# Optimization experiments

Measured on AMD Instinct MI355X. Metric: run time of the kernel, lower is better.

The kernel has to match this reference:

```python
import jax, jax.numpy as jnp
import numpy as np

B, S, D = 2, 2048, 2048
H = 16
HD = D // H
FF = 8192
EPS = 1e-5


def _layer_norm(x, g, b):
    mu = jnp.mean(x, axis=-1, keepdims=True)
    var = jnp.mean(jnp.square(x - mu), axis=-1, keepdims=True)
    return (x - mu) * jax.lax.rsqrt(var + EPS) * g + b


def setup_inputs() -> dict:
    key = jax.random.key(0)
    ks = jax.random.split(key, 8)
    s = 0.02
    return {
        "x": jax.random.normal(ks[0], (B, S, D), dtype=jnp.float32),
        "ln1_g": jnp.ones((D,), jnp.float32),
        "ln1_b": jnp.zeros((D,), jnp.float32),
        "qkv_w": jax.random.normal(ks[1], (D, 3 * D), dtype=jnp.float32) * s,
        "qkv_b": jnp.zeros((3 * D,), jnp.float32),
        "out_w": jax.random.normal(ks[2], (D, D), dtype=jnp.float32) * s,
        "out_b": jnp.zeros((D,), jnp.float32),
        "ln2_g": jnp.ones((D,), jnp.float32),
        "ln2_b": jnp.zeros((D,), jnp.float32),
        "w1": jax.random.normal(ks[3], (D, FF), dtype=jnp.float32) * s,
        "b1": jnp.zeros((FF,), jnp.float32),
        "w2": jax.random.normal(ks[4], (FF, D), dtype=jnp.float32) * s,
        "b2": jnp.zeros((D,), jnp.float32),
    }


def reference(x, ln1_g, ln1_b, qkv_w, qkv_b, out_w, out_b, ln2_g, ln2_b, w1, b1, w2, b2):
    # --- attention sub-block (pre-norm) ---
    residual = x
    h = _layer_norm(x, ln1_g, ln1_b)
    qkv = h @ qkv_w + qkv_b                      # [B,S,3D]
    q, k, v = jnp.split(qkv, 3, axis=-1)
    # [B,S,D] -> [B,H,S,HD]
    q = q.reshape(B, S, H, HD).transpose(0, 2, 1, 3)
    k = k.reshape(B, S, H, HD).transpose(0, 2, 1, 3)
    v = v.reshape(B, S, H, HD).transpose(0, 2, 1, 3)
    scores = jnp.einsum("bhqd,bhkd->bhqk", q, k)  # [B,H,S,S]
    causal = jnp.triu(jnp.ones((S, S), dtype=bool), k=1)
    scores = jnp.where(causal[None, None], -jnp.inf, scores)
    attn = jax.nn.softmax(scores / np.sqrt(HD).astype(np.float32), axis=-1)
    av = jnp.einsum("bhqk,bhkd->bhqd", attn, v)   # [B,H,S,HD]
    av = av.transpose(0, 2, 1, 3).reshape(B, S, D)
    x = residual + (av @ out_w + out_b)
    # --- FFN sub-block (pre-norm) ---
    residual = x
    h = _layer_norm(x, ln2_g, ln2_b)
    h = jax.nn.gelu(h @ w1 + b1, approximate=False)
    x = residual + (h @ w2 + b2)
    return x
```

## Files before the change

kernel.cpp:

```cpp
#include <hip/hip_runtime.h>
#include <hip/hip_bf16.h>

#define B_  2
#define S_  2048
#define D_  2048
#define H_  16
#define HD_ 128
#define FF_ 8192

typedef __bf16 bf16x8 __attribute__((ext_vector_type(8)));
typedef float  f32x4  __attribute__((ext_vector_type(4)));
typedef unsigned short u16;
typedef u16 u16x8 __attribute__((ext_vector_type(8)));
typedef unsigned uv4 __attribute__((ext_vector_type(4)));

__device__ __forceinline__ u16 f2bf(float f) {
    union { float f; unsigned u; } c; c.f = f;
    unsigned u = c.u;
    u += 0x7fffu + ((u >> 16) & 1u);
    return (u16)(u >> 16);
}

__device__ __forceinline__ void gld16(void* lds, const void* g) {
    __builtin_amdgcn_global_load_lds(
        (const __attribute__((address_space(1))) unsigned int*)g,
        (__attribute__((address_space(3))) unsigned int*)lds,
        16, 0, 0);
}

__device__ __forceinline__ bf16x8 dsr16(const u16* p) {
    unsigned a = (unsigned)(unsigned long long)
                 (const __attribute__((address_space(3))) u16*)p;
    uv4 r;
    asm volatile("ds_read_b128 %0, %1" : "=v"(r) : "v"(a));
    union { uv4 u; bf16x8 b; } c; c.u = r;
    return c.b;
}

__global__ __launch_bounds__(256)
void ln_kernel(const float* __restrict__ x, const float* __restrict__ g,
               const float* __restrict__ bb, u16* __restrict__ out)
{
    int row = blockIdx.x, tid = threadIdx.x;
    const float4* xr = (const float4*)(x + (size_t)row * D_);
    float4 a = xr[tid], c = xr[tid + 256];
    float s  = a.x + a.y + a.z + a.w + c.x + c.y + c.z + c.w;
    float s2 = a.x*a.x + a.y*a.y + a.z*a.z + a.w*a.w
             + c.x*c.x + c.y*c.y + c.z*c.z + c.w*c.w;
    #pragma unroll
    for (int off = 32; off > 0; off >>= 1) {
        s  += __shfl_down(s,  off, 64);
        s2 += __shfl_down(s2, off, 64);
    }
    __shared__ float red[16];
    __shared__ float mr[2];
    int wid = tid >> 6, lane = tid & 63;
    if (lane == 0) { red[wid] = s; red[8 + wid] = s2; }
    __syncthreads();
    if (tid == 0) {
        float ts = red[0] + red[1] + red[2] + red[3];
        float t2 = red[8] + red[9] + red[10] + red[11];
        float mu = ts * (1.0f / D_);
        float var = t2 * (1.0f / D_) - mu * mu;
        mr[0] = mu; mr[1] = rsqrtf(var + 1e-5f);
    }
    __syncthreads();
    float mu = mr[0], rstd = mr[1];
    const float4* gg = (const float4*)g;
    const float4* bv = (const float4*)bb;
    float4 g0 = gg[tid], g1 = gg[tid + 256];
    float4 b0 = bv[tid], b1 = bv[tid + 256];
    u16* orow = out + (size_t)row * D_;
    ushort4 o0, o1;
    o0.x = f2bf((a.x - mu) * rstd * g0.x + b0.x);
    o0.y = f2bf((a.y - mu) * rstd * g0.y + b0.y);
    o0.z = f2bf((a.z - mu) * rstd * g0.z + b0.z);
    o0.w = f2bf((a.w - mu) * rstd * g0.w + b0.w);
    o1.x = f2bf((c.x - mu) * rstd * g1.x + b1.x);
    o1.y = f2bf((c.y - mu) * rstd * g1.y + b1.y);
    o1.z = f2bf((c.z - mu) * rstd * g1.z + b1.z);
    o1.w = f2bf((c.w - mu) * rstd * g1.w + b1.w);
    *(ushort4*)&orow[tid * 4]         = o0;
    *(ushort4*)&orow[(tid + 256) * 4] = o1;
}

__global__ __launch_bounds__(256)
void tcvt_kernel(const float* __restrict__ W, u16* __restrict__ WT, int K, int N)
{
    __shared__ float t[32][33];
    int n0 = blockIdx.x << 5, k0 = blockIdx.y << 5;
    int tx = threadIdx.x & 31, ty = threadIdx.x >> 5;
    #pragma unroll
    for (int i = 0; i < 32; i += 8)
        t[ty + i][tx] = W[(size_t)(k0 + ty + i) * N + n0 + tx];
    __syncthreads();
    #pragma unroll
    for (int i = 0; i < 32; i += 8)
        WT[(size_t)(n0 + ty + i) * K + k0 + tx] = f2bf(t[tx][ty + i]);
}

template<int EPI>
__global__ __launch_bounds__(512, 2)
void gemm_kernel(const u16* __restrict__ A, const u16* __restrict__ BT,
                 const float* __restrict__ bias, const float* __restrict__ res,
                 void* __restrict__ outv, int M, int N, int K)
{
    __shared__ u16 ldsA[3 * 8192];
    __shared__ u16 ldsB[3 * 16384];
    (void)M;

    int tid = threadIdx.x;
    int wid = tid >> 6, lane = tid & 63;
    int wm = wid >> 2, wn = wid & 3;
    int quad = lane >> 4, l16 = lane & 15;

    int nwg = (int)gridDim.x;
    int swz = ((int)blockIdx.x & 7) * (nwg >> 3) + ((int)blockIdx.x >> 3);
    int mt = swz & 31;
    int nt = swz >> 5;
    int m0 = mt << 7, n0 = nt << 8;

    int lo3 = (tid & 7) ^ ((tid >> 3) & 7);
    int rS  = ((tid >> 3) << 1) | (lo3 >> 2);
    int cS  = (lo3 & 3) << 3;
    const u16* gA  = A  + (size_t)(m0 + rS) * K + cS;
    const u16* gB0 = BT + (size_t)(n0 + rS) * K + cS;
    const u16* gB1 = gB0 + (size_t)128 * K;

    int slot   = (((l16 & 1) << 2) | quad) ^ (l16 >> 1);
    int laneRd = (l16 >> 1) * 64 + slot * 8;
    int aRd = wm * 2048 + laneRd;
    int bRd = wn * 2048 + laneRd;

    f32x4 acc[4][4] = {};

    auto stA = [&](int b, int ks, int kofs) {
        gld16(ldsA + b * 8192 + ks * 4096 + wid * 512, gA + kofs);
    };
    auto stB = [&](int b, int ks, int kofs) {
        gld16(ldsB + b * 16384 + ks * 8192 + wid * 512, gB0 + kofs);
        gld16(ldsB + b * 16384 + ks * 8192 + 4096 + wid * 512, gB1 + kofs);
    };
    auto phase = [&](int bt, int ks, int stg, int kofs, bool vm) {
        stA(stg, ks, kofs);
        stB(stg, ks, kofs);
        const u16* ap = ldsA + bt * 8192 + ks * 4096 + aRd;
        const u16* bp = ldsB + bt * 16384 + ks * 8192 + bRd;
        bf16x8 af0 = dsr16(ap);
        bf16x8 af1 = dsr16(ap + 512);
        bf16x8 af2 = dsr16(ap + 1024);
        bf16x8 af3 = dsr16(ap + 1536);
        bf16x8 bf0 = dsr16(bp);
        bf16x8 bf1 = dsr16(bp + 512);
        bf16x8 bf2 = dsr16(bp + 1024);
        bf16x8 bf3 = dsr16(bp + 1536);
        __builtin_amdgcn_s_barrier();
        asm volatile("s_waitcnt lgkmcnt(0)" ::: "memory");
        __builtin_amdgcn_sched_barrier(0);
        __builtin_amdgcn_s_setprio(1);
        acc[0][0] = __builtin_amdgcn_mfma_f32_16x16x32_bf16(af0, bf0, acc[0][0], 0, 0, 0);
        acc[0][1] = __builtin_amdgcn_mfma_f32_16x16x32_bf16(af0, bf1, acc[0][1], 0, 0, 0);
        acc[0][2] = __builtin_amdgcn_mfma_f32_16x16x32_bf16(af0, bf2, acc[0][2], 0, 0, 0);
        acc[0][3] = __builtin_amdgcn_mfma_f32_16x16x32_bf16(af0, bf3, acc[0][3], 0, 0, 0);
        acc[1][0] = __builtin_amdgcn_mfma_f32_16x16x32_bf16(af1, bf0, acc[1][0], 0, 0, 0);
        acc[1][1] = __builtin_amdgcn_mfma_f32_16x16x32_bf16(af1, bf1, acc[1][1], 0, 0, 0);
        acc[1][2] = __builtin_amdgcn_mfma_f32_16x16x32_bf16(af1, bf2, acc[1][2], 0, 0, 0);
        acc[1][3] = __builtin_amdgcn_mfma_f32_16x16x32_bf16(af1, bf3, acc[1][3], 0, 0, 0);
        acc[2][0] = __builtin_amdgcn_mfma_f32_16x16x32_bf16(af2, bf0, acc[2][0], 0, 0, 0);
        acc[2][1] = __builtin_amdgcn_mfma_f32_16x16x32_bf16(af2, bf1, acc[2][1], 0, 0, 0);
        acc[2][2] = __builtin_amdgcn_mfma_f32_16x16x32_bf16(af2, bf2, acc[2][2], 0, 0, 0);
        acc[2][3] = __builtin_amdgcn_mfma_f32_16x16x32_bf16(af2, bf3, acc[2][3], 0, 0, 0);
        acc[3][0] = __builtin_amdgcn_mfma_f32_16x16x32_bf16(af3, bf0, acc[3][0], 0, 0, 0);
        acc[3][1] = __builtin_amdgcn_mfma_f32_16x16x32_bf16(af3, bf1, acc[3][1], 0, 0, 0);
        acc[3][2] = __builtin_amdgcn_mfma_f32_16x16x32_bf16(af3, bf2, acc[3][2], 0, 0, 0);
        acc[3][3] = __builtin_amdgcn_mfma_f32_16x16x32_bf16(af3, bf3, acc[3][3], 0, 0, 0);
        __builtin_amdgcn_sched_barrier(0);
        __builtin_amdgcn_s_setprio(0);
        if (vm) asm volatile("s_waitcnt vmcnt(6)" ::: "memory");
        __builtin_amdgcn_s_barrier();
    };

    int nkt = K >> 6;
    stA(0, 0, 0);  stB(0, 0, 0);
    stA(0, 1, 32); stB(0, 1, 32);
    stA(1, 0, 64); stB(1, 0, 64);
    stA(1, 1, 96); stB(1, 1, 96);
    asm volatile("s_waitcnt vmcnt(6)" ::: "memory");
    __builtin_amdgcn_s_barrier();

    int cur = 0;
    for (int t = 0; t < nkt; ++t) {
        int stg = cur - 1; if (stg < 0) stg = 2;
        int tp = t + 2; if (tp > nkt - 1) tp = nkt - 1;
        int kofs = tp << 6;
        phase(cur, 0, stg, kofs,      false);
        phase(cur, 1, stg, kofs + 32, true);
        cur = cur + 1; if (cur > 2) cur = 0;
    }
    asm volatile("s_waitcnt vmcnt(0)" ::: "memory");

    u16*   outb = (u16*)outv;
    float* outf = (float*)outv;
    int colb = n0 + wn * 64, rowb = m0 + wm * 64;
    #pragma unroll
    for (int j = 0; j < 4; j++) {
        int col = colb + j * 16 + l16;
        float bv = bias[col];
        #pragma unroll
        for (int i = 0; i < 4; i++) {
            int row0 = rowb + i * 16 + (quad << 2);
            #pragma unroll
            for (int r = 0; r < 4; r++) {
                float v = acc[i][j][r] + bv;
                size_t idx = (size_t)(row0 + r) * N + col;
                if (EPI == 2) {
                    outf[idx] = v + res[idx];
                } else {
                    if (EPI == 1) v = 0.5f * v * (1.0f + erff(v * 0.70710678118654752f));
                    outb[idx] = f2bf(v);
                }
            }
        }
    }
}

__global__ __launch_bounds__(256, 2)
void attn_kernel(const u16* __restrict__ qkv, u16* __restrict__ av)
{
    __shared__ u16 ldsK[4][64][32];
    __shared__ unsigned ldsVT[128][36];
    __shared__ u16 ldsP[4][32][72];
    int tid = threadIdx.x, wid = tid >> 6, lane = tid & 63;
    int quad = lane >> 4, l16 = lane & 15;
    int bh = blockIdx.y, b = bh >> 4, h = bh & 15;
    int qx = gridDim.x - 1 - blockIdx.x;
    int q0 = qx << 7;
    const u16* base = qkv + (size_t)b * S_ * (3 * D_);

    bf16x8 aq[2][4];
    #pragma unroll
    for (int set = 0; set < 2; set++) {
        int qrow = q0 + set * 64 + wid * 16 + l16;
        const u16* qp = base + (size_t)qrow * (3 * D_) + h * HD_;
        #pragma unroll
        for (int kk = 0; kk < 4; kk++)
            aq[set][kk] = *(const bf16x8*)(qp + kk * 32 + quad * 8);
    }

    float m_i[2][4], l_i[2][4];
    f32x4 oacc[2][8] = {};
    #pragma unroll
    for (int s = 0; s < 2; s++)
        #pragma unroll
        for (int r = 0; r < 4; r++) { m_i[s][r] = -1e30f; l_i[s][r] = 0.f; }

    const float scale = 0.088388347648318447f;
    int ntile = 2 * qx + 2;
    for (int jt = 0; jt < ntile; jt++) {
        int j0 = jt << 6;
        #pragma unroll
        for (int j = 0; j < 4; j++) {
            int c = wid * 4 + j;
            int kk = c >> 2, kb = c & 3;
            int key = (kb << 4) + (lane >> 2);
            const u16* g = base + (size_t)(j0 + key) * (3 * D_) + D_ + h * HD_
                         + kk * 32 + ((lane & 3) << 3);
            gld16((u16*)ldsK + c * 512, g);
        }
        {
            int kp = lane & 31, dhalf = lane >> 5;
            #pragma unroll
            for (int p = 0; p < 2; p++) {
                int doff = wid * 32 + p * 16 + dhalf * 8;
                const u16* g0 = base + (size_t)(j0 + 2 * kp) * (3 * D_)
                              + 2 * D_ + h * HD_ + doff;
                u16x8 v0 = *(const u16x8*)g0;
                u16x8 v1 = *(const u16x8*)(g0 + 3 * D_);
                #pragma unroll
                for (int k = 0; k < 8; k++)
                    ldsVT[doff + k][kp] = (unsigned)v0[k] | ((unsigned)v1[k] << 16);
            }
        }
        __syncthreads();
        f32x4 sacc[2][4] = {};
        #pragma unroll
        for (int kk = 0; kk < 4; kk++)
            #pragma unroll
            for (int n = 0; n < 4; n++) {
                bf16x8 bfr = *(const bf16x8*)&ldsK[kk][(n << 4) + l16][quad << 3];
                sacc[0][n] = __builtin_amdgcn_mfma_f32_16x16x32_bf16(aq[0][kk], bfr, sacc[0][n], 0, 0, 0);
                sacc[1][n] = __builtin_amdgcn_mfma_f32_16x16x32_bf16(aq[1][kk], bfr, sacc[1][n], 0, 0, 0);
            }
        #pragma unroll
        for (int set = 0; set < 2; set++) {
            float rowmax[4] = {-1e30f, -1e30f, -1e30f, -1e30f};
            #pragma unroll
            for (int n = 0; n < 4; n++) {
                int key = j0 + (n << 4) + l16;
                #pragma unroll
                for (int r = 0; r < 4; r++) {
                    float xv = sacc[set][n][r] * scale;
                    int qr = q0 + set * 64 + wid * 16 + (quad << 2) + r;
                    if (key > qr) xv = -1e30f;
                    sacc[set][n][r] = xv;
                    rowmax[r] = fmaxf(rowmax[r], xv);
                }
            }
            #pragma unroll
            for (int off = 1; off < 16; off <<= 1)
                #pragma unroll
                for (int r = 0; r < 4; r++)
                    rowmax[r] = fmaxf(rowmax[r], __shfl_xor(rowmax[r], off, 64));
            float alpha[4], rsum[4];
            #pragma unroll
            for (int r = 0; r < 4; r++) {
                float mn = fmaxf(m_i[set][r], rowmax[r]);
                alpha[r] = __expf(m_i[set][r] - mn);
                m_i[set][r] = mn;
                rsum[r] = 0.f;
            }
            #pragma unroll
            for (int n = 0; n < 4; n++)
                #pragma unroll
                for (int r = 0; r < 4; r++) {
                    float p = __expf(sacc[set][n][r] - m_i[set][r]);
                    rsum[r] += p;
                    ldsP[wid][set * 16 + (quad << 2) + r][(n << 4) + l16] = f2bf(p);
                }
            #pragma unroll
            for (int off = 1; off < 16; off <<= 1)
                #pragma unroll
                for (int r = 0; r < 4; r++)
                    rsum[r] += __shfl_xor(rsum[r], off, 64);
            #pragma unroll
            for (int r = 0; r < 4; r++)
                l_i[set][r] = l_i[set][r] * alpha[r] + rsum[r];
            #pragma unroll
            for (int n = 0; n < 8; n++)
                #pragma unroll
                for (int r = 0; r < 4; r++)
                    oacc[set][n][r] *= alpha[r];
        }
        #pragma unroll
        for (int ks = 0; ks < 2; ks++) {
            bf16x8 pa0 = *(const bf16x8*)&ldsP[wid][l16]     [(ks << 5) + (quad << 3)];
            bf16x8 pa1 = *(const bf16x8*)&ldsP[wid][16 + l16][(ks << 5) + (quad << 3)];
            #pragma unroll
            for (int n = 0; n < 8; n++) {
                bf16x8 vb = *(const bf16x8*)&ldsVT[(n << 4) + l16][(ks << 4) + (quad << 2)];
                oacc[0][n] = __builtin_amdgcn_mfma_f32_16x16x32_bf16(pa0, vb, oacc[0][n], 0, 0, 0);
                oacc[1][n] = __builtin_amdgcn_mfma_f32_16x16x32_bf16(pa1, vb, oacc[1][n], 0, 0, 0);
            }
        }
        __syncthreads();
    }
    #pragma unroll
    for (int set = 0; set < 2; set++)
        #pragma unroll
        for (int r = 0; r < 4; r++) {
            float inv = 1.0f / l_i[set][r];
            int qr = q0 + set * 64 + wid * 16 + (quad << 2) + r;
            u16* op = av + (size_t)(b * S_ + qr) * D_ + h * HD_;
            #pragma unroll
            for (int n = 0; n < 8; n++)
                op[(n << 4) + l16] = f2bf(oacc[set][n][r] * inv);
        }
}

extern "C" void kernel_launch(void* const* d_in, const int* in_sizes, int n_in,
                              void* d_out, int out_size, void* d_ws, size_t ws_size,
                              hipStream_t stream)
{
    const float* x     = (const float*)d_in[0];
    const float* ln1_g = (const float*)d_in[1];
    const float* ln1_b = (const float*)d_in[2];
    const float* qkv_w = (const float*)d_in[3];
    const float* qkv_b = (const float*)d_in[4];
    const float* out_w = (const float*)d_in[5];
    const float* out_b = (const float*)d_in[6];
    const float* ln2_g = (const float*)d_in[7];
    const float* ln2_b = (const float*)d_in[8];
    const float* w1    = (const float*)d_in[9];
    const float* b1    = (const float*)d_in[10];
    const float* w2    = (const float*)d_in[11];
    const float* b2    = (const float*)d_in[12];
    float* out = (float*)d_out;

    char* ws  = (char*)d_ws;
    u16* wT   = (u16*)ws;
    u16* hbuf = (u16*)(ws + (32u << 20));
    u16* big  = (u16*)(ws + (48u << 20));
    u16* qkvb = big;
    u16* ffb  = big;

    dim3 blk(256);
    dim3 gblk(512);

    ln_kernel<<<dim3(B_ * S_), blk, 0, stream>>>(x, ln1_g, ln1_b, hbuf);
    tcvt_kernel<<<dim3(6144 / 32, 2048 / 32), blk, 0, stream>>>(qkv_w, wT, 2048, 6144);
    gemm_kernel<0><<<dim3((6144 / 256) * (4096 / 128)), gblk, 0, stream>>>(
        hbuf, wT, qkv_b, nullptr, (void*)qkvb, 4096, 6144, 2048);
    attn_kernel<<<dim3(S_ / 128, B_ * H_), blk, 0, stream>>>(qkvb, hbuf);
    tcvt_kernel<<<dim3(2048 / 32, 2048 / 32), blk, 0, stream>>>(out_w, wT, 2048, 2048);
    gemm_kernel<2><<<dim3((2048 / 256) * (4096 / 128)), gblk, 0, stream>>>(
        hbuf, wT, out_b, x, (void*)out, 4096, 2048, 2048);
    ln_kernel<<<dim3(B_ * S_), blk, 0, stream>>>(out, ln2_g, ln2_b, hbuf);
    tcvt_kernel<<<dim3(8192 / 32, 2048 / 32), blk, 0, stream>>>(w1, wT, 2048, 8192);
    gemm_kernel<1><<<dim3((8192 / 256) * (4096 / 128)), gblk, 0, stream>>>(
        hbuf, wT, b1, nullptr, (void*)ffb, 4096, 8192, 2048);
    tcvt_kernel<<<dim3(2048 / 32, 8192 / 32), blk, 0, stream>>>(w2, wT, 8192, 2048);
    gemm_kernel<2><<<dim3((2048 / 256) * (4096 / 128)), gblk, 0, stream>>>(
        ffb, wT, b2, out, (void*)out, 4096, 2048, 8192);
}
```

Before: 929.0 us.

## Add 256x256 GEMM kernel for QKV/FFN1 and LDS-staged coalesced epilogues

```diff
diff --git a/kernel.cpp b/kernel.cpp
--- a/kernel.cpp
+++ b/kernel.cpp
@@ -35,6 +35,10 @@
     asm volatile("ds_read_b128 %0, %1" : "=v"(r) : "v"(a));
     union { uv4 u; bf16x8 b; } c; c.u = r;
     return c.b;
+}
+
+__device__ __forceinline__ float gelu_f(float v) {
+    return 0.5f * v * (1.0f + erff(v * 0.70710678118654752f));
 }
 
 __global__ __launch_bounds__(256)
@@ -101,12 +105,185 @@
 
 template<int EPI>
 __global__ __launch_bounds__(512, 2)
-void gemm_kernel(const u16* __restrict__ A, const u16* __restrict__ BT,
-                 const float* __restrict__ bias, const float* __restrict__ res,
-                 void* __restrict__ outv, int M, int N, int K)
+void gemm256_kernel(const u16* __restrict__ A, const u16* __restrict__ BT,
+                    const float* __restrict__ bias, const float* __restrict__ res,
+                    void* __restrict__ outv, int M, int N, int K)
 {
-    __shared__ u16 ldsA[3 * 8192];
-    __shared__ u16 ldsB[3 * 16384];
+    __shared__ u16 lds[65536];
+    u16* ldsA = lds;
+    u16* ldsB = lds + 32768;
+    (void)M; (void)res;
+
+    int tid = threadIdx.x;
+    int wid = tid >> 6, lane = tid & 63;
+    int wm = wid >> 2, wn = wid & 3;
+    int quad = lane >> 4, l16 = lane & 15;
+
+    int nwg = (int)gridDim.x;
+    int swz = ((int)blockIdx.x & 7) * (nwg >> 3) + ((int)blockIdx.x >> 3);
+    int mt = swz & 15;
+    int nt = swz >> 4;
+    int m0 = mt << 8, n0 = nt << 8;
+
+    int lo3 = (tid & 7) ^ ((tid >> 3) & 7);
+    int rS  = ((tid >> 3) << 1) | (lo3 >> 2);
+    int cS  = (lo3 & 3) << 3;
+    const u16* gA = A  + (size_t)(m0 + rS) * K + cS;
+    const u16* gB = BT + (size_t)(n0 + rS) * K + cS;
+
+    int slot   = (((l16 & 1) << 2) | quad) ^ (l16 >> 1);
+    int laneRd = (l16 >> 1) * 64 + slot * 8;
+
+    f32x4 acc[8][4] = {};
+    bf16x8 aA[4][2], aB[4][2], bfr[2][2];
+
+    auto stHalfA = [&](int bb, int h, int ko) {
+        u16* d = ldsA + bb + h * 8192 + wid * 512;
+        const u16* s = gA + (size_t)(h * 128) * K + ko;
+        gld16(d, s);
+        gld16(d + 4096, s + 32);
+    };
+    auto stHalfB = [&](int bb, int h, int ko) {
+        u16* d = ldsB + bb + h * 8192 + wid * 512;
+        const u16* s = gB + (size_t)(h * 128) * K + ko;
+        gld16(d, s);
+        gld16(d + 4096, s + 32);
+    };
+
+    #define MFMA16(AH, IOFF, JOFF)                                              \
+        __builtin_amdgcn_s_barrier();                                           \
+        asm volatile("s_waitcnt lgkmcnt(0)" ::: "memory");                      \
+        __builtin_amdgcn_sched_barrier(0);                                      \
+        __builtin_amdgcn_s_setprio(1);                                          \
+        _Pragma("unroll")                                                       \
+        for (int i = 0; i < 4; i++) {                                           \
+            _Pragma("unroll")                                                   \
+            for (int j = 0; j < 2; j++) {                                       \
+                acc[IOFF+i][JOFF+j] = __builtin_amdgcn_mfma_f32_16x16x32_bf16(  \
+                    AH[i][0], bfr[j][0], acc[IOFF+i][JOFF+j], 0, 0, 0);         \
+                acc[IOFF+i][JOFF+j] = __builtin_amdgcn_mfma_f32_16x16x32_bf16(  \
+                    AH[i][1], bfr[j][1], acc[IOFF+i][JOFF+j], 0, 0, 0);         \
+            }                                                                   \
+        }                                                                       \
+        __builtin_amdgcn_sched_barrier(0);                                      \
+        __builtin_amdgcn_s_setprio(0);                                          \
+        __builtin_amdgcn_s_barrier();
+
+    auto TILE = [&](int cb, int ob, bf16x8 (&aH0)[4][2], bf16x8 (&aH1)[4][2],
+                    int ko1, int ko2) {
+        {
+            const u16* bp = ldsB + cb + wn * 1024 + laneRd;
+            #pragma unroll
+            for (int f = 0; f < 2; f++)
+                #pragma unroll
+                for (int kk = 0; kk < 2; kk++)
+                    bfr[f][kk] = dsr16(bp + f * 512 + kk * 4096);
+            stHalfA(ob, 1, ko1);
+            MFMA16(aH0, 0, 0)
+        }
+        {
+            const u16* ap = ldsA + cb + 8192 + wm * 2048 + laneRd;
+            #pragma unroll
+            for (int f = 0; f < 4; f++)
+                #pragma unroll
+                for (int kk = 0; kk < 2; kk++)
+                    aH1[f][kk] = dsr16(ap + f * 512 + kk * 4096);
+            stHalfB(ob, 1, ko1);
+            MFMA16(aH1, 4, 0)
+        }
+        {
+            const u16* bp = ldsB + cb + 8192 + wn * 1024 + laneRd;
+            #pragma unroll
+            for (int f = 0; f < 2; f++)
+                #pragma unroll
+                for (int kk = 0; kk < 2; kk++)
+                    bfr[f][kk] = dsr16(bp + f * 512 + kk * 4096);
+            stHalfA(cb, 0, ko2);
+            MFMA16(aH1, 4, 2)
+        }
+        {
+            asm volatile("s_waitcnt vmcnt(2)" ::: "memory");
+            const u16* ap = ldsA + ob + wm * 2048 + laneRd;
+            #pragma unroll
+            for (int f = 0; f < 4; f++)
+                #pragma unroll
+                for (int kk = 0; kk < 2; kk++)
+                    aH1[f][kk] = dsr16(ap + f * 512 + kk * 4096);
+            stHalfB(cb, 0, ko2);
+            MFMA16(aH0, 0, 2)
+        }
+    };
+
+    int nkt = K >> 6;
+    stHalfA(0, 0, 0);     stHalfB(0, 0, 0);
+    stHalfA(0, 1, 0);     stHalfB(0, 1, 0);
+    stHalfA(16384, 0, 64); stHalfB(16384, 0, 64);
+    asm volatile("s_waitcnt vmcnt(4)" ::: "memory");
+    __builtin_amdgcn_s_barrier();
+    {
+        const u16* ap = ldsA + wm * 2048 + laneRd;
+        #pragma unroll
+        for (int f = 0; f < 4; f++)
+            #pragma unroll
+            for (int kk = 0; kk < 2; kk++)
+                aA[f][kk] = dsr16(ap + f * 512 + kk * 4096);
+    }
+
+    int niter = nkt >> 1;
+    for (int it = 0; it < niter; ++it) {
+        int t0 = it << 1;
+        int a1 = t0 + 1;
+        int a2 = t0 + 2; if (a2 > nkt - 1) a2 = nkt - 1;
+        int a3 = t0 + 3; if (a3 > nkt - 1) a3 = nkt - 1;
+        TILE(0,     16384, aA, aB, a1 << 6, a2 << 6);
+        TILE(16384, 0,     aB, aA, a2 << 6, a3 << 6);
+    }
+    asm volatile("s_waitcnt vmcnt(0)" ::: "memory");
+    __builtin_amdgcn_s_barrier();
+
+    u16* outb = (u16*)outv;
+    u16* bnc = lds + wid * 8192;
+    float bv[4];
+    #pragma unroll
+    for (int j = 0; j < 4; j++)
+        bv[j] = bias[n0 + (j >> 1) * 128 + wn * 32 + (j & 1) * 16 + l16];
+    #pragma unroll
+    for (int h = 0; h < 2; h++) {
+        #pragma unroll
+        for (int ii = 0; ii < 4; ii++)
+            #pragma unroll
+            for (int j = 0; j < 4; j++)
+                #pragma unroll
+                for (int r = 0; r < 4; r++) {
+                    float v = acc[h * 4 + ii][j][r] + bv[j];
+                    if (EPI == 1) v = gelu_f(v);
+                    int row = ii * 16 + (quad << 2) + r;
+                    int pc = ((j * 2 + (l16 >> 3)) ^ (row & 7));
+                    bnc[row * 64 + pc * 8 + (l16 & 7)] = f2bf(v);
+                }
+        #pragma unroll
+        for (int p = 0; p < 8; p++) {
+            int brow = p * 8 + (lane >> 3);
+            int ch = lane & 7;
+            int phys = ch ^ (brow & 7);
+            u16x8 v8 = *(const u16x8*)&bnc[brow * 64 + phys * 8];
+            int grow = m0 + h * 128 + wm * 64 + brow;
+            int gcol = n0 + (ch >> 2) * 128 + wn * 32 + (ch & 3) * 8;
+            *(u16x8*)&outb[(size_t)grow * N + gcol] = v8;
+        }
+        __builtin_amdgcn_s_barrier();
+    }
+    #undef MFMA16
+}
+
+__global__ __launch_bounds__(512, 2)
+void gemm128_kernel(const u16* __restrict__ A, const u16* __restrict__ BT,
+                    const float* __restrict__ bias, const float* __restrict__ res,
+                    float* __restrict__ outf, int M, int N, int K)
+{
+    __shared__ u16 lds[73728];
+    u16* ldsA = lds;
+    u16* ldsB = lds + 24576;
     (void)M;
 
     int tid = threadIdx.x;
@@ -198,29 +375,35 @@
         cur = cur + 1; if (cur > 2) cur = 0;
     }
     asm volatile("s_waitcnt vmcnt(0)" ::: "memory");
-
-    u16*   outb = (u16*)outv;
-    float* outf = (float*)outv;
+    __builtin_amdgcn_s_barrier();
+
+    float* bnc = (float*)lds + wid * 4096;
     int colb = n0 + wn * 64, rowb = m0 + wm * 64;
-    #pragma unroll
-    for (int j = 0; j < 4; j++) {
-        int col = colb + j * 16 + l16;
-        float bv = bias[col];
-        #pragma unroll
-        for (int i = 0; i < 4; i++) {
-            int row0 = rowb + i * 16 + (quad << 2);
+    float bv[4];
+    #pragma unroll
+    for (int j = 0; j < 4; j++) bv[j] = bias[colb + j * 16 + l16];
+    #pragma unroll
+    for (int i = 0; i < 4; i++)
+        #pragma unroll
+        for (int j = 0; j < 4; j++)
             #pragma unroll
             for (int r = 0; r < 4; r++) {
-                float v = acc[i][j][r] + bv;
-                size_t idx = (size_t)(row0 + r) * N + col;
-                if (EPI == 2) {
-                    outf[idx] = v + res[idx];
-                } else {
-                    if (EPI == 1) v = 0.5f * v * (1.0f + erff(v * 0.70710678118654752f));
-                    outb[idx] = f2bf(v);
-                }
+                int row = i * 16 + (quad << 2) + r;
+                int col = j * 16 + l16;
+                int c = col >> 2, lo2 = col & 3;
+                int pc = c ^ (row & 7);
+                bnc[row * 64 + pc * 4 + lo2] = acc[i][j][r] + bv[j];
             }
-        }
+    #pragma unroll
+    for (int p = 0; p < 16; p++) {
+        int brow = p * 4 + (lane >> 4);
+        int cl = lane & 15;
+        int phys = cl ^ (brow & 7);
+        f32x4 v4 = *(const f32x4*)&bnc[brow * 64 + phys * 4];
+        size_t idx = (size_t)(rowb + brow) * N + colb + cl * 4;
+        f32x4 r4 = *(const f32x4*)&res[idx];
+        v4 += r4;
+        *(f32x4*)&outf[idx] = v4;
     }
 }
 
@@ -398,17 +581,17 @@
 
     ln_kernel<<<dim3(B_ * S_), blk, 0, stream>>>(x, ln1_g, ln1_b, hbuf);
     tcvt_kernel<<<dim3(6144 / 32, 2048 / 32), blk, 0, stream>>>(qkv_w, wT, 2048, 6144);
-    gemm_kernel<0><<<dim3((6144 / 256) * (4096 / 128)), gblk, 0, stream>>>(
+    gemm256_kernel<0><<<dim3((6144 / 256) * (4096 / 256)), gblk, 0, stream>>>(
         hbuf, wT, qkv_b, nullptr, (void*)qkvb, 4096, 6144, 2048);
     attn_kernel<<<dim3(S_ / 128, B_ * H_), blk, 0, stream>>>(qkvb, hbuf);
     tcvt_kernel<<<dim3(2048 / 32, 2048 / 32), blk, 0, stream>>>(out_w, wT, 2048, 2048);
-    gemm_kernel<2><<<dim3((2048 / 256) * (4096 / 128)), gblk, 0, stream>>>(
-        hbuf, wT, out_b, x, (void*)out, 4096, 2048, 2048);
+    gemm128_kernel<<<dim3((2048 / 256) * (4096 / 128)), gblk, 0, stream>>>(
+        hbuf, wT, out_b, x, out, 4096, 2048, 2048);
     ln_kernel<<<dim3(B_ * S_), blk, 0, stream>>>(out, ln2_g, ln2_b, hbuf);
     tcvt_kernel<<<dim3(8192 / 32, 2048 / 32), blk, 0, stream>>>(w1, wT, 2048, 8192);
-    gemm_kernel<1><<<dim3((8192 / 256) * (4096 / 128)), gblk, 0, stream>>>(
+    gemm256_kernel<1><<<dim3((8192 / 256) * (4096 / 256)), gblk, 0, stream>>>(
         hbuf, wT, b1, nullptr, (void*)ffb, 4096, 8192, 2048);
     tcvt_kernel<<<dim3(2048 / 32, 8192 / 32), blk, 0, stream>>>(w2, wT, 8192, 2048);
-    gemm_kernel<2><<<dim3((2048 / 256) * (4096 / 128)), gblk, 0, stream>>>(
-        ffb, wT, b2, out, (void*)out, 4096, 2048, 8192);
-}
+    gemm128_kernel<<<dim3((2048 / 256) * (4096 / 128)), gblk, 0, stream>>>(
+        ffb, wT, b2, out, out, 4096, 2048, 8192);
+}
```

Measured after the change: 1.006 ms. +8.3%, slower.
